# Kernel optimization log

Hardware: AMD Instinct MI355X
Metric: run time of the kernel (lower is better)

Reference implementation:

```python
import jax, jax.numpy as jnp
import numpy as np
from functools import partial

V, BS, L, H, C = 50257, 1024, 6, 12, 768
HD = C // H

def _ln(x, w, b):
    mu = jnp.mean(x, axis=-1, keepdims=True)
    var = jnp.var(x, axis=-1, keepdims=True)
    return (x - mu) * jax.lax.rsqrt(var + 1e-5) * w + b

def setup_inputs() -> dict:
    key = jax.random.key(0)
    ks = jax.random.split(key, 12)
    s = 0.02
    inp = {
        "idx": jax.random.randint(ks[0], (4, 1024), 0, V, dtype=jnp.int32),
        "wte": jax.random.normal(ks[1], (V, C), jnp.float32) * s,
        "wpe": jax.random.normal(ks[2], (BS, C), jnp.float32) * s,
        # per-block stacked params; linear weights stored [in, out]
        "ln1_w": jnp.ones((L, C)), "ln1_b": jnp.zeros((L, C)),
        "attn_w": jax.random.normal(ks[3], (L, C, 3 * C), jnp.float32) * s,
        "attn_b": jnp.zeros((L, 3 * C)),
        "proj_w": jax.random.normal(ks[4], (L, C, C), jnp.float32) * s,
        "proj_b": jnp.zeros((L, C)),
        "ln2_w": jnp.ones((L, C)), "ln2_b": jnp.zeros((L, C)),
        "fc_w": jax.random.normal(ks[5], (L, C, 4 * C), jnp.float32) * s,
        "fc_b": jnp.zeros((L, 4 * C)),
        "fc2_w": jax.random.normal(ks[6], (L, 4 * C, C), jnp.float32) * s,
        "fc2_b": jnp.zeros((L, C)),
        "lnf_w": jnp.ones((C,)), "lnf_b": jnp.zeros((C,)),
    }
    return inp

def _forward(idx, wte, wpe, ln1_w, ln1_b, attn_w, attn_b, proj_w, proj_b,
             ln2_w, ln2_b, fc_w, fc_b, fc2_w, fc2_b, lnf_w, lnf_b):
    B, T = idx.shape
    x = wte[idx] + wpe[:T]  # [B,T,C]
    causal = jnp.tril(jnp.ones((T, T), bool))  # [T,T]
    scale = 1.0 / np.sqrt(HD)
    neg_inf = jnp.finfo(x.dtype).min

    def block(x, p):
        l1w, l1b, aw, ab, pw, pb, l2w, l2b, fw, fb, f2w, f2b = p
        h = _ln(x, l1w, l1b)
        qkv = h @ aw + ab  # [B,T,3C]
        q, k, v = jnp.split(qkv, 3, axis=-1)
        q = q.reshape(B, T, H, HD)
        k = k.reshape(B, T, H, HD)
        v = v.reshape(B, T, H, HD)
        att = jnp.einsum('bqhd,bkhd->bhqk', q, k) * scale
        att = jnp.where(causal, att, neg_inf)
        att = jax.nn.softmax(att, axis=-1)
        y = jnp.einsum('bhqk,bkhd->bqhd', att, v).reshape(B, T, C)
        x = x + y @ pw + pb
        h = _ln(x, l2w, l2b)
        h = jax.nn.gelu(h @ fw + fb, approximate=False)  # torch nn.GELU default = exact
        x = x + h @ f2w + f2b
        return x, None

    params = (ln1_w, ln1_b, attn_w, attn_b, proj_w, proj_b,
              ln2_w, ln2_b, fc_w, fc_b, fc2_w, fc2_b)
    x, _ = jax.lax.scan(block, x, params)
    x = _ln(x, lnf_w, lnf_b)
    logits = x @ wte.T  # tied lm_head, no bias
    return logits

def reference(idx, wte, wpe, ln1_w, ln1_b, attn_w, attn_b, proj_w, proj_b,
              ln2_w, ln2_b, fc_w, fc_b, fc2_w, fc2_b, lnf_w, lnf_b):
    return _forward(idx, wte, wpe, ln1_w, ln1_b, attn_w, attn_b, proj_w, proj_b,
                    ln2_w, ln2_b, fc_w, fc_b, fc2_w, fc2_b, lnf_w, lnf_b)
```

## Files before the change

### kernel.cpp

```cpp
#include <hip/hip_runtime.h>

#define BT     4096
#define CDIM   768
#define NLAYER 6
#define NHEAD  12
#define VREAL  50257
#define VPAD   50432

typedef __bf16 bf16x8 __attribute__((ext_vector_type(8)));
typedef float  f32x4  __attribute__((ext_vector_type(4)));

__device__ __forceinline__ unsigned short f2bf(float f) {
    unsigned int u = __builtin_bit_cast(unsigned int, f);
    u += 0x7fffu + ((u >> 16) & 1u);
    return (unsigned short)(u >> 16);
}

__device__ __forceinline__ void gload16(const unsigned short* g, unsigned short* l) {
    __builtin_amdgcn_global_load_lds(
        (const __attribute__((address_space(1))) unsigned int*)g,
        (__attribute__((address_space(3))) unsigned int*)l, 16, 0, 0);
}

__device__ __forceinline__ void swz_block(int &bx, int &by) {
    int gx = gridDim.x;
    int nwg = gx * gridDim.y;
    if ((nwg & 7) == 0) {
        int lin = by * gx + bx;
        int q = nwg >> 3;
        lin = (lin & 7) * q + (lin >> 3);
        bx = lin % gx;
        by = lin / gx;
    }
}

__global__ __launch_bounds__(256) void transpose_conv(
    const float* __restrict__ in, unsigned short* __restrict__ out, int K, int N)
{
    in  += (size_t)blockIdx.z * K * N;
    out += (size_t)blockIdx.z * K * N;
    __shared__ float t[32][33];
    int j0 = blockIdx.x * 32;
    int i0 = blockIdx.y * 32;
    int c = threadIdx.x;
    int r = threadIdx.y;
    #pragma unroll
    for (int rr = r; rr < 32; rr += 8)
        t[rr][c] = in[(size_t)(i0 + rr) * N + j0 + c];
    __syncthreads();
    #pragma unroll
    for (int rr = r; rr < 32; rr += 8)
        out[(size_t)(j0 + rr) * K + i0 + c] = f2bf(t[c][rr]);
}

__global__ __launch_bounds__(256) void wteconv(
    const float* __restrict__ wte, unsigned short* __restrict__ out)
{
    size_t e = ((size_t)blockIdx.x * 256 + threadIdx.x) * 4;
    int row = (int)(e / CDIM);
    int col = (int)(e % CDIM);
    ushort4 o;
    if (row < VREAL) {
        float4 v = *(const float4*)(wte + (size_t)row * CDIM + col);
        o.x = f2bf(v.x); o.y = f2bf(v.y); o.z = f2bf(v.z); o.w = f2bf(v.w);
    } else {
        o.x = 0; o.y = 0; o.z = 0; o.w = 0;
    }
    *(ushort4*)(out + e) = o;
}

__global__ __launch_bounds__(256) void embed_kernel(
    const int* __restrict__ idx, const float* __restrict__ wte,
    const float* __restrict__ wpe, float* __restrict__ x)
{
    int row = blockIdx.x;
    int t = row & 1023;
    int id = idx[row];
    const float* s = wte + (size_t)id * CDIM;
    const float* p = wpe + (size_t)t * CDIM;
    float* o = x + (size_t)row * CDIM;
    for (int c = threadIdx.x; c < CDIM; c += 256) o[c] = s[c] + p[c];
}

__global__ __launch_bounds__(256) void ln_kernel(
    const float* __restrict__ x, const float* __restrict__ w,
    const float* __restrict__ b, unsigned short* __restrict__ out)
{
    int row = blockIdx.x * 4 + (threadIdx.x >> 6);
    int lane = threadIdx.x & 63;
    const float* xp = x + (size_t)row * CDIM;
    float v[12];
    float s = 0.f, sq = 0.f;
    #pragma unroll
    for (int j = 0; j < 12; ++j) {
        float t = xp[j * 64 + lane];
        v[j] = t; s += t; sq += t * t;
    }
    #pragma unroll
    for (int o = 32; o > 0; o >>= 1) {
        s  += __shfl_xor(s, o, 64);
        sq += __shfl_xor(sq, o, 64);
    }
    float mu  = s * (1.f / CDIM);
    float var = sq * (1.f / CDIM) - mu * mu;
    float rs  = rsqrtf(var + 1e-5f);
    unsigned short* op = out + (size_t)row * CDIM;
    #pragma unroll
    for (int j = 0; j < 12; ++j) {
        int c = j * 64 + lane;
        op[c] = f2bf((v[j] - mu) * rs * w[c] + b[c]);
    }
}

template<int MODE>
__global__ __launch_bounds__(256) void gemm_kernel(
    const unsigned short* __restrict__ A, const unsigned short* __restrict__ Bt,
    const float* __restrict__ bias, const float* __restrict__ resid,
    float* __restrict__ outF, unsigned short* __restrict__ outB,
    unsigned short* __restrict__ qout, unsigned short* __restrict__ kout,
    unsigned short* __restrict__ vtout,
    int K, int Nout)
{
    __shared__ alignas(16) unsigned short As[4096];
    __shared__ alignas(16) unsigned short Bs[4096];
    const int tid  = threadIdx.x;
    const int wv   = tid >> 6;
    const int lane = tid & 63;
    const int m0 = blockIdx.x * 128;
    const int n0 = blockIdx.y * 128;
    const int wr = wv >> 1, wc = wv & 1;
    const int srow = lane >> 2;
    const int skk  = (lane & 3) * 8;
    const int fr = lane & 15;
    const int fk = (lane >> 4) * 8;

    f32x4 acc[4][4];
    #pragma unroll
    for (int i = 0; i < 4; ++i)
        #pragma unroll
        for (int j = 0; j < 4; ++j) acc[i][j] = f32x4{0.f, 0.f, 0.f, 0.f};

    for (int k0 = 0; k0 < K; k0 += 32) {
        #pragma unroll
        for (int j = 0; j < 2; ++j) {
            int row = j * 64 + wv * 16 + srow;
            gload16(A  + (size_t)(m0 + row) * K + k0 + skk, &As[j * 2048 + wv * 512]);
            gload16(Bt + (size_t)(n0 + row) * K + k0 + skk, &Bs[j * 2048 + wv * 512]);
        }
        __syncthreads();
        bf16x8 a[4], bb[4];
        #pragma unroll
        for (int m = 0; m < 4; ++m)
            a[m] = *(const bf16x8*)&As[(wr * 64 + m * 16 + fr) * 32 + fk];
        #pragma unroll
        for (int n = 0; n < 4; ++n)
            bb[n] = *(const bf16x8*)&Bs[(wc * 64 + n * 16 + fr) * 32 + fk];
        #pragma unroll
        for (int m = 0; m < 4; ++m)
            #pragma unroll
            for (int n = 0; n < 4; ++n)
                acc[m][n] = __builtin_amdgcn_mfma_f32_16x16x32_bf16(
                    a[m], bb[n], acc[m][n], 0, 0, 0);
        __syncthreads();
    }

    const int colb = n0 + wc * 64 + fr;
    const int rowb = m0 + wr * 64 + (lane >> 4) * 4;
    #pragma unroll
    for (int m = 0; m < 4; ++m) {
        #pragma unroll
        for (int n = 0; n < 4; ++n) {
            int col = colb + n * 16;
            int which = col / 768;
            int hh = (col - which * 768) >> 6;
            int dd = col & 63;
            #pragma unroll
            for (int r = 0; r < 4; ++r) {
                int row = rowb + m * 16 + r;
                float v = acc[m][n][r];
                if (MODE == 1) {
                    outF[(size_t)row * Nout + col] =
                        resid[(size_t)row * Nout + col] + v + bias[col];
                } else if (MODE == 2) {
                    float u = v + bias[col];
                    float g = 0.5f * u * (1.f + erff(u * 0.70710678118654752f));
                    outB[(size_t)row * Nout + col] = f2bf(g);
                } else if (MODE == 4) {
                    int bb2 = row >> 10, tt = row & 1023;
                    unsigned short val = f2bf(v + bias[col]);
                    if (which == 0)
                        qout[(((size_t)bb2 * NHEAD + hh) * 1024 + tt) * 64 + dd] = val;
                    else if (which == 1)
                        kout[(((size_t)bb2 * NHEAD + hh) * 1024 + tt) * 64 + dd] = val;
                    else
                        vtout[(((size_t)bb2 * NHEAD + hh) * 64 + dd) * 1024 + tt] = val;
                }
            }
        }
    }
}

__global__ __launch_bounds__(256, 2) void lmhead_kernel(
    const unsigned short* __restrict__ A, const unsigned short* __restrict__ Bt,
    float* __restrict__ outF)
{
    __shared__ alignas(16) unsigned short ldsA[2][8192];
    const int tid  = threadIdx.x;
    const int wv   = tid >> 6;
    const int lane = tid & 63;
    const int fr = lane & 15, fg = lane >> 4;
    int bx = blockIdx.x, by = blockIdx.y;
    swz_block(bx, by);
    const int m0 = blockIdx.z * 2048 + bx * 128;
    const int n0 = by * 256;

    const int srow = wv * 8 + (lane >> 3);
    const int sks  = ((lane & 7) * 8) ^ ((lane >> 3) << 3);

    const unsigned short* Bw = Bt + (size_t)(n0 + wv * 64 + fr) * 768 + fg * 8;

    const int swz0 = (fg * 8) ^ ((fr & 7) << 3);
    const int swz1 = (32 + fg * 8) ^ ((fr & 7) << 3);

    f32x4 acc[8][4];
    #pragma unroll
    for (int m = 0; m < 8; ++m)
        #pragma unroll
        for (int n = 0; n < 4; ++n) acc[m][n] = f32x4{0.f, 0.f, 0.f, 0.f};

    bf16x8 brE[4][2], brO[4][2];

#define LM_STAGE_A(t, buf)                                                    \
    {                                                                         \
        const int k0_ = (t) * 64;                                             \
        _Pragma("unroll")                                                     \
        for (int j = 0; j < 4; ++j)                                           \
            gload16(A + (size_t)(m0 + j * 32 + srow) * 768 + k0_ + sks,       \
                    &ldsA[buf][j * 2048 + wv * 512]);                         \
    }
#define LM_LOAD_B(t, br)                                                      \
    {                                                                         \
        const int k0_ = (t) * 64;                                             \
        _Pragma("unroll")                                                     \
        for (int nf = 0; nf < 4; ++nf) {                                      \
            br[nf][0] = *(const bf16x8*)(Bw + (size_t)nf * 16 * 768 + k0_);   \
            br[nf][1] = *(const bf16x8*)(Bw + (size_t)nf * 16 * 768 + k0_ + 32); \
        }                                                                     \
    }
#define LM_COMPUTE(buf, br)                                                   \
    {                                                                         \
        _Pragma("unroll")                                                     \
        for (int m = 0; m < 8; ++m) {                                         \
            bf16x8 a0 = *(const bf16x8*)&ldsA[buf][(m * 16 + fr) * 64 + swz0];\
            bf16x8 a1 = *(const bf16x8*)&ldsA[buf][(m * 16 + fr) * 64 + swz1];\
            _Pragma("unroll")                                                 \
            for (int nf = 0; nf < 4; ++nf) {                                  \
                acc[m][nf] = __builtin_amdgcn_mfma_f32_16x16x32_bf16(a0, br[nf][0], acc[m][nf], 0, 0, 0); \
                acc[m][nf] = __builtin_amdgcn_mfma_f32_16x16x32_bf16(a1, br[nf][1], acc[m][nf], 0, 0, 0); \
            }                                                                 \
        }                                                                     \
    }

    LM_STAGE_A(0, 0);
    LM_LOAD_B(0, brE);

    #pragma unroll 1
    for (int tt = 0; tt < 12; tt += 2) {
        LM_STAGE_A(tt + 1, 1);
        LM_LOAD_B(tt + 1, brO);
        asm volatile("s_waitcnt vmcnt(12)" ::: "memory");
        __builtin_amdgcn_s_barrier();
        __builtin_amdgcn_s_setprio(1);
        LM_COMPUTE(0, brE);
        __builtin_amdgcn_s_setprio(0);
        asm volatile("s_waitcnt lgkmcnt(0)" ::: "memory");
        __builtin_amdgcn_sched_barrier(0);
        __builtin_amdgcn_s_barrier();
        if (tt + 2 < 12) {
            LM_STAGE_A(tt + 2, 0);
            LM_LOAD_B(tt + 2, brE);
            asm volatile("s_waitcnt vmcnt(12)" ::: "memory");
        } else {
            asm volatile("s_waitcnt vmcnt(0)" ::: "memory");
        }
        __builtin_amdgcn_s_barrier();
        __builtin_amdgcn_s_setprio(1);
        LM_COMPUTE(1, brO);
        __builtin_amdgcn_s_setprio(0);
        asm volatile("s_waitcnt lgkmcnt(0)" ::: "memory");
        __builtin_amdgcn_sched_barrier(0);
        __builtin_amdgcn_s_barrier();
    }
#undef LM_STAGE_A
#undef LM_LOAD_B
#undef LM_COMPUTE

    const int colb = n0 + wv * 64 + fr;
    const int rowb = m0 + fg * 4;
    #pragma unroll
    for (int m = 0; m < 8; ++m) {
        #pragma unroll
        for (int n = 0; n < 4; ++n) {
            int col = colb + n * 16;
            if (col < VREAL) {
                #pragma unroll
                for (int r = 0; r < 4; ++r) {
                    int row = rowb + m * 16 + r;
                    outF[(size_t)row * VREAL + col] = acc[m][n][r];
                }
            }
        }
    }
}

__global__ __launch_bounds__(256) void attn_mfma_kernel(
    const unsigned short* __restrict__ qb, const unsigned short* __restrict__ kb,
    const unsigned short* __restrict__ vtb, unsigned short* __restrict__ y)
{
    __shared__ alignas(16) unsigned short Ps[4][16][72];
    const int qt = 15 - blockIdx.x;
    const int h = blockIdx.y, b = blockIdx.z;
    const int w = threadIdx.x >> 6, lane = threadIdx.x & 63;
    const int fr = lane & 15;
    const int fg = lane >> 4;
    const size_t bh = (size_t)(b * NHEAD + h);
    const unsigned short* Qb = qb  + bh * 1024 * 64;
    const unsigned short* Kb = kb  + bh * 1024 * 64;
    const unsigned short* Vt = vtb + bh * 64 * 1024;
    const int q0 = qt * 64 + w * 16;

    bf16x8 aq[2];
    aq[0] = *(const bf16x8*)(Qb + (size_t)(q0 + fr) * 64 + fg * 8);
    aq[1] = *(const bf16x8*)(Qb + (size_t)(q0 + fr) * 64 + 32 + fg * 8);

    f32x4 o[4];
    #pragma unroll
    for (int c = 0; c < 4; ++c) o[c] = f32x4{0.f, 0.f, 0.f, 0.f};
    float m[4], l[4];
    #pragma unroll
    for (int r = 0; r < 4; ++r) { m[r] = -1e30f; l[r] = 0.f; }

    for (int kt = 0; kt <= qt; ++kt) {
        const unsigned short* Kt = Kb + (size_t)kt * 64 * 64;
        f32x4 s[4];
        #pragma unroll
        for (int c = 0; c < 4; ++c) {
            bf16x8 bk0 = *(const bf16x8*)(Kt + (size_t)(c * 16 + fr) * 64 + fg * 8);
            bf16x8 bk1 = *(const bf16x8*)(Kt + (size_t)(c * 16 + fr) * 64 + 32 + fg * 8);
            s[c] = f32x4{0.f, 0.f, 0.f, 0.f};
            s[c] = __builtin_amdgcn_mfma_f32_16x16x32_bf16(aq[0], bk0, s[c], 0, 0, 0);
            s[c] = __builtin_amdgcn_mfma_f32_16x16x32_bf16(aq[1], bk1, s[c], 0, 0, 0);
        }
        float sc[4][4];
        #pragma unroll
        for (int c = 0; c < 4; ++c)
            #pragma unroll
            for (int r = 0; r < 4; ++r) {
                float v = s[c][r] * 0.125f;
                if (kt == qt && (kt * 64 + c * 16 + fr) > (q0 + fg * 4 + r))
                    v = -1e30f;
                sc[c][r] = v;
            }
        #pragma unroll
        for (int r = 0; r < 4; ++r) {
            float tm = fmaxf(fmaxf(sc[0][r], sc[1][r]), fmaxf(sc[2][r], sc[3][r]));
            tm = fmaxf(tm, __shfl_xor(tm, 1, 64));
            tm = fmaxf(tm, __shfl_xor(tm, 2, 64));
            tm = fmaxf(tm, __shfl_xor(tm, 4, 64));
            tm = fmaxf(tm, __shfl_xor(tm, 8, 64));
            float mn = fmaxf(m[r], tm);
            float corr = __expf(m[r] - mn);
            m[r] = mn;
            float ps = 0.f;
            #pragma unroll
            for (int c = 0; c < 4; ++c) {
                float p = __expf(sc[c][r] - mn);
                sc[c][r] = p;
                ps += p;
            }
            ps += __shfl_xor(ps, 1, 64);
            ps += __shfl_xor(ps, 2, 64);
            ps += __shfl_xor(ps, 4, 64);
            ps += __shfl_xor(ps, 8, 64);
            l[r] = l[r] * corr + ps;
            #pragma unroll
            for (int c = 0; c < 4; ++c) o[c][r] *= corr;
            #pragma unroll
            for (int c = 0; c < 4; ++c)
                Ps[w][fg * 4 + r][c * 16 + fr] = f2bf(sc[c][r]);
        }
        asm volatile("s_waitcnt lgkmcnt(0)" ::: "memory");
        bf16x8 ap0 = *(const bf16x8*)&Ps[w][fr][fg * 8];
        bf16x8 ap1 = *(const bf16x8*)&Ps[w][fr][32 + fg * 8];
        #pragma unroll
        for (int c = 0; c < 4; ++c) {
            const unsigned short* vb = Vt + (size_t)(c * 16 + fr) * 1024 + kt * 64;
            bf16x8 bv0 = *(const bf16x8*)(vb + fg * 8);
            bf16x8 bv1 = *(const bf16x8*)(vb + 32 + fg * 8);
            o[c] = __builtin_amdgcn_mfma_f32_16x16x32_bf16(ap0, bv0, o[c], 0, 0, 0);
            o[c] = __builtin_amdgcn_mfma_f32_16x16x32_bf16(ap1, bv1, o[c], 0, 0, 0);
        }
        asm volatile("s_waitcnt lgkmcnt(0)" ::: "memory");
    }

    float inv[4];
    #pragma unroll
    for (int r = 0; r < 4; ++r) inv[r] = 1.f / l[r];
    #pragma unroll
    for (int c = 0; c < 4; ++c)
        #pragma unroll
        for (int r = 0; r < 4; ++r) {
            int q = q0 + fg * 4 + r;
            y[((size_t)(b * 1024 + q)) * CDIM + h * 64 + c * 16 + fr] =
                f2bf(o[c][r] * inv[r]);
        }
}

extern "C" void kernel_launch(void* const* d_in, const int* in_sizes, int n_in,
                              void* d_out, int out_size, void* d_ws, size_t ws_size,
                              hipStream_t stream) {
    (void)in_sizes; (void)n_in; (void)out_size; (void)ws_size;
    const int*   idx   = (const int*)  d_in[0];
    const float* wte   = (const float*)d_in[1];
    const float* wpe   = (const float*)d_in[2];
    const float* ln1w  = (const float*)d_in[3];
    const float* ln1b  = (const float*)d_in[4];
    const float* attnw = (const float*)d_in[5];
    const float* attnb = (const float*)d_in[6];
    const float* projw = (const float*)d_in[7];
    const float* projb = (const float*)d_in[8];
    const float* ln2w  = (const float*)d_in[9];
    const float* ln2b  = (const float*)d_in[10];
    const float* fcw   = (const float*)d_in[11];
    const float* fcb   = (const float*)d_in[12];
    const float* fc2w  = (const float*)d_in[13];
    const float* fc2b  = (const float*)d_in[14];
    const float* lnfw  = (const float*)d_in[15];
    const float* lnfb  = (const float*)d_in[16];
    float* out = (float*)d_out;

    char* ws = (char*)d_ws;
    size_t off = 0;
    auto alloc = [&](size_t bytes) {
        void* p = ws + off;
        off += (bytes + 255) & ~(size_t)255;
        return p;
    };
    float*          x      = (float*)         alloc((size_t)BT * CDIM * 4);
    unsigned short* hbuf   = (unsigned short*)alloc((size_t)BT * CDIM * 2);
    unsigned short* qbuf   = (unsigned short*)alloc((size_t)BT * CDIM * 2);
    unsigned short* kbuf   = (unsigned short*)alloc((size_t)BT * CDIM * 2);
    unsigned short* vtbuf  = (unsigned short*)alloc((size_t)BT * CDIM * 2);
    unsigned short* ybuf   = (unsigned short*)alloc((size_t)BT * CDIM * 2);
    unsigned short* fcact  = (unsigned short*)alloc((size_t)BT * 4 * CDIM * 2);
    unsigned short* wqkvT  = (unsigned short*)alloc((size_t)NLAYER * 3 * CDIM * CDIM * 2);
    unsigned short* wprojT = (unsigned short*)alloc((size_t)NLAYER * CDIM * CDIM * 2);
    unsigned short* wfcT   = (unsigned short*)alloc((size_t)NLAYER * 4 * CDIM * CDIM * 2);
    unsigned short* wfc2T  = (unsigned short*)alloc((size_t)NLAYER * 4 * CDIM * CDIM * 2);
    unsigned short* wteB   = (unsigned short*)alloc((size_t)VPAD * CDIM * 2);

    transpose_conv<<<dim3(3*CDIM/32,   CDIM/32, NLAYER), dim3(32,8), 0, stream>>>(attnw, wqkvT, CDIM, 3*CDIM);
    transpose_conv<<<dim3(  CDIM/32,   CDIM/32, NLAYER), dim3(32,8), 0, stream>>>(projw, wprojT, CDIM, CDIM);
    transpose_conv<<<dim3(4*CDIM/32,   CDIM/32, NLAYER), dim3(32,8), 0, stream>>>(fcw,  wfcT,  CDIM, 4*CDIM);
    transpose_conv<<<dim3(  CDIM/32, 4*CDIM/32, NLAYER), dim3(32,8), 0, stream>>>(fc2w, wfc2T, 4*CDIM, CDIM);
    wteconv<<<(VPAD * CDIM / 4) / 256, 256, 0, stream>>>(wte, wteB);
    embed_kernel<<<BT, 256, 0, stream>>>(idx, wte, wpe, x);

    for (int l = 0; l < NLAYER; ++l) {
        ln_kernel<<<BT/4, 256, 0, stream>>>(x, ln1w + l*CDIM, ln1b + l*CDIM, hbuf);
        gemm_kernel<4><<<dim3(BT/128, 3*CDIM/128), 256, 0, stream>>>(
            hbuf, wqkvT + (size_t)l*3*CDIM*CDIM, attnb + (size_t)l*3*CDIM,
            nullptr, nullptr, nullptr, qbuf, kbuf, vtbuf, CDIM, 3*CDIM);
        attn_mfma_kernel<<<dim3(16, NHEAD, 4), 256, 0, stream>>>(qbuf, kbuf, vtbuf, ybuf);
        gemm_kernel<1><<<dim3(BT/128, CDIM/128), 256, 0, stream>>>(
            ybuf, wprojT + (size_t)l*CDIM*CDIM, projb + (size_t)l*CDIM,
            x, x, nullptr, nullptr, nullptr, nullptr, CDIM, CDIM);
        ln_kernel<<<BT/4, 256, 0, stream>>>(x, ln2w + l*CDIM, ln2b + l*CDIM, hbuf);
        gemm_kernel<2><<<dim3(BT/128, 4*CDIM/128), 256, 0, stream>>>(
            hbuf, wfcT + (size_t)l*4*CDIM*CDIM, fcb + (size_t)l*4*CDIM,
            nullptr, nullptr, fcact, nullptr, nullptr, nullptr, CDIM, 4*CDIM);
        gemm_kernel<1><<<dim3(BT/128, CDIM/128), 256, 0, stream>>>(
            fcact, wfc2T + (size_t)l*4*CDIM*CDIM, fc2b + (size_t)l*CDIM,
            x, x, nullptr, nullptr, nullptr, nullptr, 4*CDIM, CDIM);
    }
    ln_kernel<<<BT/4, 256, 0, stream>>>(x, lnfw, lnfb, hbuf);
    lmhead_kernel<<<dim3(16, VPAD/256, 2), 256, 0, stream>>>(hbuf, wteB, out);
}
```

Before: 2.355 ms.

## Use 64x64-tile GEMM for residual projections and skip softmax rescale when max unchanged

Adds a 64x64 output-tile MFMA GEMM kernel for the two N=768 residual GEMMs (attention projection and FC2). The old 128x128 tiling launched only 192 blocks, and the smaller tile raises that to 768 blocks so all CUs have work. The trade is less data reuse per block and a simple single-buffered K loop with two barriers per 32-wide K step. In attention, the online-softmax correction of the running sum and accumulator now runs only when the row max grows, saving exp and multiply work. That adds a branch that can diverge.

```diff
diff --git a/kernel.cpp b/kernel.cpp
--- a/kernel.cpp
+++ b/kernel.cpp
@@ -200,6 +200,68 @@
     }
 }
 
+__global__ __launch_bounds__(256) void gemm64_kernel(
+    const unsigned short* __restrict__ A, const unsigned short* __restrict__ Bt,
+    const float* __restrict__ bias, const float* __restrict__ resid,
+    float* __restrict__ outF, int K, int Nout)
+{
+    __shared__ alignas(16) unsigned short As[2048];
+    __shared__ alignas(16) unsigned short Bs[2048];
+    const int tid  = threadIdx.x;
+    const int wv   = tid >> 6;
+    const int lane = tid & 63;
+    const int m0 = blockIdx.x * 64;
+    const int n0 = blockIdx.y * 64;
+    const int wr = wv >> 1, wc = wv & 1;
+    const int srow = lane >> 2;
+    const int skk  = (lane & 3) * 8;
+    const int fr = lane & 15;
+    const int fk = (lane >> 4) * 8;
+
+    f32x4 acc[2][2];
+    #pragma unroll
+    for (int i = 0; i < 2; ++i)
+        #pragma unroll
+        for (int j = 0; j < 2; ++j) acc[i][j] = f32x4{0.f, 0.f, 0.f, 0.f};
+
+    for (int k0 = 0; k0 < K; k0 += 32) {
+        int row = wv * 16 + srow;
+        gload16(A  + (size_t)(m0 + row) * K + k0 + skk, &As[wv * 512]);
+        gload16(Bt + (size_t)(n0 + row) * K + k0 + skk, &Bs[wv * 512]);
+        __syncthreads();
+        bf16x8 a[2], bb[2];
+        #pragma unroll
+        for (int m = 0; m < 2; ++m)
+            a[m] = *(const bf16x8*)&As[(wr * 32 + m * 16 + fr) * 32 + fk];
+        #pragma unroll
+        for (int n = 0; n < 2; ++n)
+            bb[n] = *(const bf16x8*)&Bs[(wc * 32 + n * 16 + fr) * 32 + fk];
+        #pragma unroll
+        for (int m = 0; m < 2; ++m)
+            #pragma unroll
+            for (int n = 0; n < 2; ++n)
+                acc[m][n] = __builtin_amdgcn_mfma_f32_16x16x32_bf16(
+                    a[m], bb[n], acc[m][n], 0, 0, 0);
+        __syncthreads();
+    }
+
+    const int colb = n0 + wc * 32 + fr;
+    const int rowb = m0 + wr * 32 + (lane >> 4) * 4;
+    #pragma unroll
+    for (int m = 0; m < 2; ++m) {
+        #pragma unroll
+        for (int n = 0; n < 2; ++n) {
+            int col = colb + n * 16;
+            #pragma unroll
+            for (int r = 0; r < 4; ++r) {
+                int row = rowb + m * 16 + r;
+                outF[(size_t)row * Nout + col] =
+                    resid[(size_t)row * Nout + col] + acc[m][n][r] + bias[col];
+            }
+        }
+    }
+}
+
 __global__ __launch_bounds__(256, 2) void lmhead_kernel(
     const unsigned short* __restrict__ A, const unsigned short* __restrict__ Bt,
     float* __restrict__ outF)
@@ -368,13 +430,17 @@
             tm = fmaxf(tm, __shfl_xor(tm, 2, 64));
             tm = fmaxf(tm, __shfl_xor(tm, 4, 64));
             tm = fmaxf(tm, __shfl_xor(tm, 8, 64));
-            float mn = fmaxf(m[r], tm);
-            float corr = __expf(m[r] - mn);
-            m[r] = mn;
+            if (tm > m[r]) {
+                float corr = __expf(m[r] - tm);
+                m[r] = tm;
+                l[r] *= corr;
+                #pragma unroll
+                for (int c = 0; c < 4; ++c) o[c][r] *= corr;
+            }
             float ps = 0.f;
             #pragma unroll
             for (int c = 0; c < 4; ++c) {
-                float p = __expf(sc[c][r] - mn);
+                float p = __expf(sc[c][r] - m[r]);
                 sc[c][r] = p;
                 ps += p;
             }
@@ -382,9 +448,7 @@
             ps += __shfl_xor(ps, 2, 64);
             ps += __shfl_xor(ps, 4, 64);
             ps += __shfl_xor(ps, 8, 64);
-            l[r] = l[r] * corr + ps;
-            #pragma unroll
-            for (int c = 0; c < 4; ++c) o[c][r] *= corr;
+            l[r] += ps;
             #pragma unroll
             for (int c = 0; c < 4; ++c)
                 Ps[w][fg * 4 + r][c * 16 + fr] = f2bf(sc[c][r]);
@@ -472,16 +536,16 @@
             hbuf, wqkvT + (size_t)l*3*CDIM*CDIM, attnb + (size_t)l*3*CDIM,
             nullptr, nullptr, nullptr, qbuf, kbuf, vtbuf, CDIM, 3*CDIM);
         attn_mfma_kernel<<<dim3(16, NHEAD, 4), 256, 0, stream>>>(qbuf, kbuf, vtbuf, ybuf);
-        gemm_kernel<1><<<dim3(BT/128, CDIM/128), 256, 0, stream>>>(
+        gemm64_kernel<<<dim3(BT/64, CDIM/64), 256, 0, stream>>>(
             ybuf, wprojT + (size_t)l*CDIM*CDIM, projb + (size_t)l*CDIM,
-            x, x, nullptr, nullptr, nullptr, nullptr, CDIM, CDIM);
+            x, x, CDIM, CDIM);
         ln_kernel<<<BT/4, 256, 0, stream>>>(x, ln2w + l*CDIM, ln2b + l*CDIM, hbuf);
         gemm_kernel<2><<<dim3(BT/128, 4*CDIM/128), 256, 0, stream>>>(
             hbuf, wfcT + (size_t)l*4*CDIM*CDIM, fcb + (size_t)l*4*CDIM,
             nullptr, nullptr, fcact, nullptr, nullptr, nullptr, CDIM, 4*CDIM);
-        gemm_kernel<1><<<dim3(BT/128, CDIM/128), 256, 0, stream>>>(
+        gemm64_kernel<<<dim3(BT/64, CDIM/64), 256, 0, stream>>>(
             fcact, wfc2T + (size_t)l*4*CDIM*CDIM, fc2b + (size_t)l*CDIM,
-            x, x, nullptr, nullptr, nullptr, nullptr, 4*CDIM, CDIM);
+            x, x, 4*CDIM, CDIM);
     }
     ln_kernel<<<BT/4, 256, 0, stream>>>(x, lnfw, lnfb, hbuf);
     lmhead_kernel<<<dim3(16, VPAD/256, 2), 256, 0, stream>>>(hbuf, wteB, out);
```

After: 2.192 ms. -6.9%, faster.
